# Kernel optimization log

Hardware: AMD Instinct MI355X
Metric: run time of the kernel (lower is better)

## Reference

```python
import jax, jax.numpy as jnp
import numpy as np


def _diag_perm(h, w):
    # Matches torch loop: offsets -(h-1)..w-1, within offset ordered by row i.
    ii, jj = np.meshgrid(np.arange(h), np.arange(w), indexing='ij')
    idx = np.lexsort((ii.ravel(), (jj - ii).ravel())).astype(np.int32)
    inv = np.argsort(idx).astype(np.int32)
    return jnp.asarray(idx), jnp.asarray(inv)


def _mamba(tok, ln_g, ln_b, Win, conv_w, conv_b, Wx, Wdt, bdt, A_log, Dp, Wout):
    # tok: (B, L, C). MambaLayer = LayerNorm + standard Mamba block.
    di, dc = conv_w.shape
    ds = A_log.shape[-1]
    dtr = Wdt.shape[-1]
    mu = tok.mean(-1, keepdims=True)
    var = ((tok - mu) ** 2).mean(-1, keepdims=True)
    t = (tok - mu) * jax.lax.rsqrt(var + 1e-5) * ln_g + ln_b
    xz = jnp.einsum('blc,ec->ble', t, Win)          # (B,L,2*di)
    xh, z = jnp.split(xz, 2, axis=-1)
    # causal depthwise conv over sequence
    xc = jnp.transpose(xh, (0, 2, 1))               # (B,di,L)
    xc = jax.lax.conv_general_dilated(
        xc, conv_w[:, None, :], (1,), [(dc - 1, 0)],
        dimension_numbers=('NCH', 'OIH', 'NCH'), feature_group_count=di)
    u = jax.nn.silu(jnp.transpose(xc, (0, 2, 1)) + conv_b)  # (B,L,di)
    proj = jnp.einsum('bld,ed->ble', u, Wx)
    dt_r, Bm, Cm = jnp.split(proj, [dtr, dtr + ds], axis=-1)
    dt = jax.nn.softplus(jnp.einsum('blr,dr->bld', dt_r, Wdt) + bdt)  # (B,L,di)
    A = -jnp.exp(A_log)                              # (di,ds)

    def step(h, inp):
        dt_t, B_t, C_t, u_t = inp                    # (B,di) (B,ds) (B,ds) (B,di)
        dA = jnp.exp(dt_t[..., None] * A)            # (B,di,ds)
        h = dA * h + dt_t[..., None] * B_t[:, None, :] * u_t[..., None]
        y = jnp.einsum('bds,bs->bd', h, C_t)
        return h, y

    h0 = jnp.zeros((u.shape[0], di, ds), u.dtype)
    _, ys = jax.lax.scan(step, h0, (jnp.moveaxis(dt, 1, 0), jnp.moveaxis(Bm, 1, 0),
                                    jnp.moveaxis(Cm, 1, 0), jnp.moveaxis(u, 1, 0)))
    y = jnp.moveaxis(ys, 0, 1) + u * Dp              # (B,L,di)
    y = y * jax.nn.silu(z)
    return jnp.einsum('bld,cd->blc', y, Wout)


def _forward(x, ln_g, ln_b, Win, conv_w, conv_b, Wx, Wdt, bdt, A_log, Dp, Wout):
    b, c, h, w = x.shape
    idx, inv = _diag_perm(h, w)

    def mam(d, tok):
        return _mamba(tok, ln_g[d], ln_b[d], Win[d], conv_w[d], conv_b[d],
                      Wx[d], Wdt[d], bdt[d], A_log[d], Dp[d], Wout[d])

    row_tok = x.reshape(b, c, h * w).transpose(0, 2, 1)
    row_feat = mam(0, row_tok).transpose(0, 2, 1).reshape(b, c, h, w)
    col_tok = x.transpose(0, 1, 3, 2).reshape(b, c, w * h).transpose(0, 2, 1)
    col_feat = mam(1, col_tok).transpose(0, 2, 1).reshape(b, c, w, h).transpose(0, 1, 3, 2)
    diag_feat = mam(2, row_tok[:, idx, :])[:, inv, :].transpose(0, 2, 1).reshape(b, c, h, w)
    xf = x[:, :, :, ::-1]
    anti_tok = xf.reshape(b, c, h * w).transpose(0, 2, 1)[:, idx, :]
    anti_feat = mam(3, anti_tok)[:, inv, :].transpose(0, 2, 1).reshape(b, c, h, w)[:, :, :, ::-1]
    gate = jax.nn.sigmoid((row_feat + col_feat + diag_feat + anti_feat) / 4.0)
    return x * gate


def setup_inputs() -> dict:
    key = jax.random.key(0)
    ks = jax.random.split(key, 8)
    B, C, H, W = 4, 96, 48, 48
    DI, DS, DC, DTR = 192, 16, 4, 6
    s = 0.05
    return {
        'x': jax.random.normal(ks[0], (B, C, H, W), jnp.float32),
        'ln_g': jnp.ones((4, C), jnp.float32),
        'ln_b': jnp.zeros((4, C), jnp.float32),
        'Win': jax.random.normal(ks[1], (4, 2 * DI, C), jnp.float32) * s,
        'conv_w': jax.random.normal(ks[2], (4, DI, DC), jnp.float32) * s,
        'conv_b': jnp.zeros((4, DI), jnp.float32),
        'Wx': jax.random.normal(ks[3], (4, DTR + 2 * DS, DI), jnp.float32) * s,
        'Wdt': jax.random.normal(ks[4], (4, DI, DTR), jnp.float32) * s,
        'bdt': jax.random.normal(ks[5], (4, DI), jnp.float32) * s,
        'A_log': jnp.log(jnp.broadcast_to(jnp.arange(1, DS + 1, dtype=jnp.float32), (4, DI, DS))),
        'Dp': jnp.ones((4, DI), jnp.float32),
        'Wout': jax.random.normal(ks[6], (4, C, DI), jnp.float32) * s,
    }


def reference(x, ln_g, ln_b, Win, conv_w, conv_b, Wx, Wdt, bdt, A_log, Dp, Wout):
    return _forward(x, ln_g, ln_b, Win, conv_w, conv_b, Wx, Wdt, bdt, A_log, Dp, Wout)
```

## Files before the change

kernel.cpp:

```cpp
#include <hip/hip_runtime.h>
#include <math.h>

#define LSEQ 2304
#define LC 32
#define NCH 72

typedef unsigned short u16;
typedef unsigned int u32;
typedef __attribute__((ext_vector_type(8))) short bf16x8;
typedef __attribute__((ext_vector_type(4))) float f32x4;

__device__ __forceinline__ float sigmoidf_(float v){ return 1.f/(1.f+__expf(-v)); }
__device__ __forceinline__ u16 f2b(float f){
  union{float f; u32 u;} v; v.f = f;
  u32 r = v.u + 0x7fffu + ((v.u >> 16) & 1u);
  return (u16)(r >> 16);
}
__device__ __forceinline__ float b2f(u16 h){
  union{u32 u; float f;} v; v.u = ((u32)h) << 16; return v.f;
}
__device__ __forceinline__ u16 f2h(float f){
  _Float16 h = (_Float16)f;
  union{_Float16 h; u16 u;} v; v.h = h; return v.u;
}
__device__ __forceinline__ float h2f(u16 u){
  union{u16 u; _Float16 h;} v; v.u = u; return (float)v.h;
}
__device__ __forceinline__ uint2 pack4(float a, float b, float c, float d){
  uint2 o;
  o.x = (u32)f2b(a) | ((u32)f2b(b) << 16);
  o.y = (u32)f2b(c) | ((u32)f2b(d) << 16);
  return o;
}
__device__ __forceinline__ float softplus_(float v){
  return fmaxf(v, 0.f) + __logf(1.f + __expf(-fabsf(v)));
}

__global__ void g_kernel(int* __restrict__ g, int* __restrict__ flag){
  int tid = threadIdx.x;
  if (tid == 0) *flag = 1;
  for (int l = tid; l < LSEQ; l += 256){
    g[l] = l;
    g[LSEQ + l] = (l % 48) * 48 + l / 48;
  }
  for (int p = tid; p < LSEQ; p += 256){
    int i = p / 48, j = p % 48, dd = j - i;
    int off = (dd <= 0) ? (47 + dd) * (48 + dd) / 2
                        : 1176 + 48 * (dd - 1) - dd * (dd - 1) / 2;
    int l = off + min(i, j);
    g[2 * LSEQ + l] = p;
  }
  __syncthreads();
  for (int l = tid; l < LSEQ; l += 256){
    int p2 = g[2 * LSEQ + l];
    g[3 * LSEQ + l] = (p2 / 48) * 48 + 47 - (p2 % 48);
  }
}

__global__ void prep_fold(const float* __restrict__ Win, const float* __restrict__ ln_g,
                          const float* __restrict__ ln_b, const float* __restrict__ A_log,
                          const float* __restrict__ Wout, const float* __restrict__ Wx,
                          const float* __restrict__ Wdt, const float* __restrict__ bdt,
                          u16* __restrict__ WinMF, float* __restrict__ b2,
                          float* __restrict__ Aneg2, u16* __restrict__ WoutMF,
                          u16* __restrict__ Wcomb, float* __restrict__ bcomb,
                          int* __restrict__ flag){
  int i = blockIdx.x * 256 + threadIdx.x;
  if (i < 4*192*16){
    float a = -expf(A_log[i]);
    Aneg2[i] = a * 1.44269504f;
    int s = i & 15;
    float a0 = -expf(A_log[i - s]);
    if (fabsf(a - (float)(s + 1) * a0) > 1e-5f * fabsf(a) + 1e-30f)
      atomicAnd(flag, 0);
  }
  if (i < 4*384*96){
    int d = i / 36864, r = i % 36864, c = r % 96;
    WinMF[i] = f2b(Win[i] * ln_g[d*96 + c]);
  }
  if (i < 4*96*192) WoutMF[i] = f2b(Wout[i]);
  if (i < 4*224*192){
    int d = i / 43008, r = i % 43008, e = r / 192, c = r % 192;
    float w;
    if (e < 192){
      const float* wdt = &Wdt[(size_t)(d*192 + e) * 6];
      w = 0.f;
      #pragma unroll
      for (int r6 = 0; r6 < 6; ++r6) w += wdt[r6] * Wx[(size_t)(d*38 + r6) * 192 + c];
    } else if (e < 208){
      w = Wx[(size_t)(d*38 + 6 + (e - 192)) * 192 + c];
    } else {
      w = Wx[(size_t)(d*38 + 22 + (e - 208)) * 192 + c];
    }
    Wcomb[i] = f2b(w);
  }
  if (i < 4*224){
    int d = i / 224, e = i % 224;
    bcomb[i] = (e < 192) ? bdt[d*192 + e] : 0.f;
  }
  if (i < 4*384){
    int d = i / 384;
    const float* wr = &Win[(size_t)i * 96];
    const float* lb = &ln_b[d * 96];
    float s = 0.f;
    for (int c = 0; c < 96; ++c) s += wr[c] * lb[c];
    b2[i] = s;
  }
}

__global__ __launch_bounds__(256) void ln_kernel(const float* __restrict__ x, u16* __restrict__ n){
  __shared__ float red[512];
  int tid = threadIdx.x;
  int s = tid & 63, q = tid >> 6;
  int T = blockIdx.x * 64 + s;
  int b = T / 2304, p = T % 2304;
  const float* xp = x + (size_t)b * 96 * 2304 + p;
  float vals[24];
  float sum = 0.f, ss = 0.f;
  #pragma unroll
  for (int k = 0; k < 24; ++k){
    float v = xp[(size_t)(q*24 + k) * 2304];
    vals[k] = v; sum += v; ss += v*v;
  }
  red[q*64 + s] = sum;
  red[256 + q*64 + s] = ss;
  __syncthreads();
  float S = red[s] + red[64+s] + red[128+s] + red[192+s];
  float Q = red[256+s] + red[320+s] + red[384+s] + red[448+s];
  float mu = S * (1.f/96.f);
  float var = Q * (1.f/96.f) - mu*mu;
  float rs = rsqrtf(var + 1e-5f);
  u32 w[12];
  #pragma unroll
  for (int k = 0; k < 12; ++k){
    float v0 = (vals[2*k]   - mu) * rs;
    float v1 = (vals[2*k+1] - mu) * rs;
    w[k] = (u32)f2b(v0) | ((u32)f2b(v1) << 16);
  }
  uint4* np_ = (uint4*)(n + (size_t)T * 96 + q*24);
  np_[0] = make_uint4(w[0], w[1], w[2],  w[3]);
  np_[1] = make_uint4(w[4], w[5], w[6],  w[7]);
  np_[2] = make_uint4(w[8], w[9], w[10], w[11]);
}

__global__ __launch_bounds__(256) void kproj(const u16* __restrict__ nbf,
    const u16* __restrict__ WinMF, const float* __restrict__ b2,
    u16* __restrict__ xz){
  int d = blockIdx.y;
  int wv = threadIdx.x >> 6, lane = threadIdx.x & 63;
  int lr = lane & 15, lg = lane >> 4;
  int r0 = blockIdx.x * 64 + wv * 16;
  const u16* Ap = nbf + (size_t)(r0 + lr) * 96 + lg * 8;
  bf16x8 tk0 = *(const bf16x8*)(Ap);
  bf16x8 tk1 = *(const bf16x8*)(Ap + 32);
  bf16x8 tk2 = *(const bf16x8*)(Ap + 64);
  const u16* Wb = WinMF + (size_t)d * 36864 + (size_t)lr * 96 + lg * 8;
  const float* b2d = b2 + d * 384;
  u16* out = xz + ((size_t)d * 9216 + r0 + lr) * 384;
  for (int grp = 0; grp < 3; ++grp){
    f32x4 acc[8];
    #pragma unroll
    for (int t = 0; t < 8; ++t)
      acc[t] = *(const f32x4*)&b2d[(grp*8 + t)*16 + lg*4];
    #pragma unroll
    for (int t = 0; t < 8; ++t){
      const u16* wp = Wb + (size_t)(grp*8 + t) * 1536;
      acc[t] = __builtin_amdgcn_mfma_f32_16x16x32_bf16(*(const bf16x8*)(wp     ), tk0, acc[t], 0, 0, 0);
      acc[t] = __builtin_amdgcn_mfma_f32_16x16x32_bf16(*(const bf16x8*)(wp + 32), tk1, acc[t], 0, 0, 0);
      acc[t] = __builtin_amdgcn_mfma_f32_16x16x32_bf16(*(const bf16x8*)(wp + 64), tk2, acc[t], 0, 0, 0);
    }
    #pragma unroll
    for (int t = 0; t < 8; ++t){
      uint2 o = pack4(acc[t][0], acc[t][1], acc[t][2], acc[t][3]);
      *(uint2*)&out[(grp*8 + t)*16 + lg*4] = o;
    }
  }
}

__global__ __launch_bounds__(256) void kconv(const u16* __restrict__ xz, const int* __restrict__ g,
    const float* __restrict__ conv_w, const float* __restrict__ conv_b,
    u16* __restrict__ u, u16* __restrict__ sz){
  __shared__ u16 xh[67][200];
  int d = blockIdx.z, b = blockIdx.y, l0 = blockIdx.x * 64;
  int tid = threadIdx.x;
  const int* gd = g + d * LSEQ;
  const u16* xzd = xz + (size_t)d * 9216 * 384 + (size_t)b * LSEQ * 384;
  for (int i = tid; i < 67*24; i += 256){
    int lt = i / 24, j = i % 24;
    int gl = l0 - 3 + lt;
    uint4 v = make_uint4(0u, 0u, 0u, 0u);
    if (gl >= 0){
      int p = gd[gl];
      v = *(const uint4*)(xzd + (size_t)p * 384 + j * 8);
    }
    *(uint4*)&xh[lt][j*8] = v;
  }
  size_t obase = ((size_t)(d*4 + b) * LSEQ + l0) * 192;
  for (int i = tid; i < 64*48; i += 256){
    int lt = i / 48, j = (i % 48) * 4;
    int p = gd[l0 + lt];
    uint2 zv = *(const uint2*)(xzd + (size_t)p * 384 + 192 + j);
    float z0 = b2f((u16)(zv.x & 0xffff)), z1 = b2f((u16)(zv.x >> 16));
    float z2 = b2f((u16)(zv.y & 0xffff)), z3 = b2f((u16)(zv.y >> 16));
    z0 *= sigmoidf_(z0); z1 *= sigmoidf_(z1); z2 *= sigmoidf_(z2); z3 *= sigmoidf_(z3);
    *(uint2*)(sz + obase + (size_t)lt * 192 + j) = pack4(z0, z1, z2, z3);
  }
  __syncthreads();
  for (int i = tid; i < 64*48; i += 256){
    int lt = i / 48, j = (i % 48) * 4;
    float a0 = conv_b[d*192 + j + 0];
    float a1 = conv_b[d*192 + j + 1];
    float a2 = conv_b[d*192 + j + 2];
    float a3 = conv_b[d*192 + j + 3];
    const float4 w0 = *(const float4*)&conv_w[(size_t)(d*192 + j + 0) * 4];
    const float4 w1 = *(const float4*)&conv_w[(size_t)(d*192 + j + 1) * 4];
    const float4 w2 = *(const float4*)&conv_w[(size_t)(d*192 + j + 2) * 4];
    const float4 w3 = *(const float4*)&conv_w[(size_t)(d*192 + j + 3) * 4];
    const float* w0p = (const float*)&w0;
    const float* w1p = (const float*)&w1;
    const float* w2p = (const float*)&w2;
    const float* w3p = (const float*)&w3;
    #pragma unroll
    for (int kk = 0; kk < 4; ++kk){
      uint2 xv = *(const uint2*)&xh[lt + kk][j];
      a0 += w0p[kk] * b2f((u16)(xv.x & 0xffff));
      a1 += w1p[kk] * b2f((u16)(xv.x >> 16));
      a2 += w2p[kk] * b2f((u16)(xv.y & 0xffff));
      a3 += w3p[kk] * b2f((u16)(xv.y >> 16));
    }
    a0 *= sigmoidf_(a0); a1 *= sigmoidf_(a1); a2 *= sigmoidf_(a2); a3 *= sigmoidf_(a3);
    *(uint2*)(u + obase + (size_t)lt * 192 + j) = pack4(a0, a1, a2, a3);
  }
}

__global__ __launch_bounds__(256) void kernBM(const u16* __restrict__ u,
    const u16* __restrict__ Wcomb, const float* __restrict__ bcomb,
    u16* __restrict__ dtb, float* __restrict__ Bm, float* __restrict__ Cm){
  __shared__ u16 ush[64 * 200];
  int d = blockIdx.y;
  int tid = threadIdx.x;
  int tile0 = blockIdx.x * 64;
  const u16* ub = u + ((size_t)d * 4 * LSEQ + tile0) * 192;
  for (int i = tid; i < 64*24; i += 256){
    int row = i / 24, c8 = i % 24;
    *(uint4*)&ush[row*200 + c8*8] = *(const uint4*)&ub[(size_t)row*192 + c8*8];
  }
  __syncthreads();
  int wv = tid >> 6, lane = tid & 63;
  int lr = lane & 15, lg = lane >> 4;
  const u16* urow = &ush[(wv*16 + lr)*200 + lg*8];
  bf16x8 tk[6];
  #pragma unroll
  for (int kc = 0; kc < 6; ++kc) tk[kc] = *(const bf16x8*)(urow + kc*32);
  const u16* Wb = Wcomb + (size_t)d * 224 * 192 + (size_t)lr * 192 + lg * 8;
  bf16x8 bw[2][6];
  #pragma unroll
  for (int kc = 0; kc < 6; ++kc) bw[0][kc] = *(const bf16x8*)(Wb + kc*32);
  size_t tokrow = (size_t)d * 4 * LSEQ + tile0 + wv*16 + lr;
  for (int t = 0; t < 14; ++t){
    int cur = t & 1;
    if (t < 13){
      const u16* wp = Wb + (size_t)(t + 1) * 3072;
      #pragma unroll
      for (int kc = 0; kc < 6; ++kc) bw[cur^1][kc] = *(const bf16x8*)(wp + kc*32);
    }
    f32x4 a = (f32x4){0.f, 0.f, 0.f, 0.f};
    #pragma unroll
    for (int kc = 0; kc < 6; ++kc)
      a = __builtin_amdgcn_mfma_f32_16x16x32_bf16(bw[cur][kc], tk[kc], a, 0, 0, 0);
    if (t < 12){
      f32x4 bb = *(const f32x4*)&bcomb[d*224 + t*16 + lg*4];
      float s0 = softplus_(a[0] + bb[0]);
      float s1 = softplus_(a[1] + bb[1]);
      float s2 = softplus_(a[2] + bb[2]);
      float s3 = softplus_(a[3] + bb[3]);
      uint2 o;
      o.x = (u32)f2h(s0) | ((u32)f2h(s1) << 16);
      o.y = (u32)f2h(s2) | ((u32)f2h(s3) << 16);
      *(uint2*)&dtb[tokrow * 192 + t*16 + lg*4] = o;
    } else if (t == 12){
      *(float4*)&Bm[tokrow * 16 + lg*4] = make_float4(a[0], a[1], a[2], a[3]);
    } else {
      *(float4*)&Cm[tokrow * 16 + lg*4] = make_float4(a[0], a[1], a[2], a[3]);
    }
  }
}

__global__ __launch_bounds__(192) void kernC1(const u16* __restrict__ dtb, const u16* __restrict__ u,
    const float* __restrict__ Bm, const float* __restrict__ Cm,
    const float* __restrict__ Aneg2, const int* __restrict__ flag,
    u16* __restrict__ hfin, float* __restrict__ Send, u32* __restrict__ yS){
  __shared__ float Bsh[LC*16];
  __shared__ float Csh[LC*16];
  int ch = blockIdx.x, b = blockIdx.y, d = blockIdx.z;
  int seq = d*4 + b;
  int di = threadIdx.x;
  size_t tb = (size_t)seq * LSEQ + ch * LC;
  const float* bp = Bm + tb * 16;
  const float* cp = Cm + tb * 16;
  for (int i = di; i < LC*16; i += 192){ Bsh[i] = bp[i]; Csh[i] = cp[i]; }
  const u16* dtp = dtb + tb * 192;
  const u16* up  = u   + tb * 192;
  u32* ySp = yS + tb * 192;
  float h[16];
  #pragma unroll
  for (int s = 0; s < 16; ++s) h[s] = 0.f;
  float Sacc = 0.f;
  __syncthreads();
  if (*flag){
    float A2_0 = Aneg2[(d*192 + di) * 16];
    for (int j = 0; j < LC; ++j){
      float dtv = h2f(dtp[j*192 + di]);
      float uv  = b2f(up[j*192 + di]);
      float Bs[16], Cs[16];
      {
        const float4* b4 = (const float4*)&Bsh[j * 16];
        const float4* c4 = (const float4*)&Csh[j * 16];
        #pragma unroll
        for (int q = 0; q < 4; ++q){
          float4 v = b4[q]; Bs[q*4]=v.x; Bs[q*4+1]=v.y; Bs[q*4+2]=v.z; Bs[q*4+3]=v.w;
          float4 w = c4[q]; Cs[q*4]=w.x; Cs[q*4+1]=w.y; Cs[q*4+2]=w.z; Cs[q*4+3]=w.w;
        }
      }
      float dtu = dtv * uv;
      float e1 = __builtin_amdgcn_exp2f(dtv * A2_0);
      float e2 = e1*e1, e4 = e2*e2, e8 = e4*e4;
      float p[8];
      p[0]=e1; p[1]=e2; p[2]=e1*e2; p[3]=e4; p[4]=e1*e4; p[5]=e2*e4; p[6]=p[2]*e4; p[7]=e8;
      float yv = 0.f;
      #pragma unroll
      for (int s = 0; s < 8; ++s){
        h[s] = p[s]*h[s] + dtu*Bs[s];
        yv += h[s]*Cs[s];
        float q = p[s]*e8;
        h[s+8] = q*h[s+8] + dtu*Bs[s+8];
        yv += h[s+8]*Cs[s+8];
      }
      Sacc += dtv;
      ySp[j*192 + di] = (u32)f2h(yv) | ((u32)f2h(Sacc) << 16);
    }
  } else {
    float A2[16];
    {
      const float4* ap = (const float4*)&Aneg2[(d*192 + di) * 16];
      #pragma unroll
      for (int q = 0; q < 4; ++q){ float4 a4 = ap[q]; A2[q*4]=a4.x; A2[q*4+1]=a4.y; A2[q*4+2]=a4.z; A2[q*4+3]=a4.w; }
    }
    for (int j = 0; j < LC; ++j){
      float dtv = h2f(dtp[j*192 + di]);
      float uv  = b2f(up[j*192 + di]);
      float Bs[16], Cs[16];
      {
        const float4* b4 = (const float4*)&Bsh[j * 16];
        const float4* c4 = (const float4*)&Csh[j * 16];
        #pragma unroll
        for (int q = 0; q < 4; ++q){
          float4 v = b4[q]; Bs[q*4]=v.x; Bs[q*4+1]=v.y; Bs[q*4+2]=v.z; Bs[q*4+3]=v.w;
          float4 w = c4[q]; Cs[q*4]=w.x; Cs[q*4+1]=w.y; Cs[q*4+2]=w.z; Cs[q*4+3]=w.w;
        }
      }
      float dtu = dtv * uv;
      float yv = 0.f;
      #pragma unroll
      for (int s = 0; s < 16; ++s){
        h[s] = __builtin_amdgcn_exp2f(dtv * A2[s]) * h[s] + dtu * Bs[s];
        yv += h[s] * Cs[s];
      }
      Sacc += dtv;
      ySp[j*192 + di] = (u32)f2h(yv) | ((u32)f2h(Sacc) << 16);
    }
  }
  u16* hf = &hfin[((size_t)seq * NCH + ch) * 3072 + di * 16];
  uint4 o0, o1;
  o0.x = (u32)f2b(h[0])  | ((u32)f2b(h[1])  << 16);
  o0.y = (u32)f2b(h[2])  | ((u32)f2b(h[3])  << 16);
  o0.z = (u32)f2b(h[4])  | ((u32)f2b(h[5])  << 16);
  o0.w = (u32)f2b(h[6])  | ((u32)f2b(h[7])  << 16);
  o1.x = (u32)f2b(h[8])  | ((u32)f2b(h[9])  << 16);
  o1.y = (u32)f2b(h[10]) | ((u32)f2b(h[11]) << 16);
  o1.z = (u32)f2b(h[12]) | ((u32)f2b(h[13]) << 16);
  o1.w = (u32)f2b(h[14]) | ((u32)f2b(h[15]) << 16);
  *(uint4*)hf = o0;
  *(uint4*)(hf + 8) = o1;
  Send[((size_t)seq * NCH + ch) * 192 + di] = Sacc;
}

__global__ __launch_bounds__(256) void kernC2(const u16* __restrict__ hfin, const float* __restrict__ Send,
    const float* __restrict__ Aneg2, u16* __restrict__ hin){
  int t = blockIdx.x * 256 + threadIdx.x;
  int seq = t / 3072, q = t % 3072;
  int di = q >> 4, s = q & 15;
  int d = seq >> 2;
  float A2 = Aneg2[(d*192 + di)*16 + s];
  float hr = 0.f;
  const u16* hf = hfin + (size_t)seq * NCH * 3072 + q;
  u16* hi = hin + (size_t)seq * NCH * 3072 + q;
  const float* Se = Send + (size_t)seq * NCH * 192 + di;
  for (int ch = 0; ch < NCH; ++ch){
    hi[(size_t)ch * 3072] = f2b(hr);
    hr = b2f(hf[(size_t)ch * 3072]) + __builtin_amdgcn_exp2f(A2 * Se[(size_t)ch * 192]) * hr;
  }
}

__global__ __launch_bounds__(384) void kscan2out(const u32* __restrict__ yS, const u16* __restrict__ u,
    const float* __restrict__ Cm,
    const float* __restrict__ Aneg2, const int* __restrict__ flag, const u16* __restrict__ hin,
    const u16* __restrict__ sz, const float* __restrict__ Dp,
    const u16* __restrict__ WoutMF, const int* __restrict__ g,
    u16* __restrict__ feat){
  __shared__ float Csh[64*16];
  __shared__ u16 vsh[64][200];
  int b = blockIdx.y, d = blockIdx.z;
  int seq = d*4 + b;
  int l0 = blockIdx.x * 64;
  int tid = threadIdx.x;
  int gc = tid / 192, di = tid % 192;
  int ch = blockIdx.x * 2 + gc;
  {
    const float* cp = Cm + ((size_t)seq * LSEQ + l0) * 16;
    for (int i = tid; i < 64*16; i += 384) Csh[i] = cp[i];
  }
  float hs[16];
  {
    const uint4* hi4 = (const uint4*)&hin[((size_t)seq * NCH + ch) * 3072 + di * 16];
    uint4 v0 = hi4[0], v1 = hi4[1];
    hs[0]=b2f((u16)(v0.x&0xffff)); hs[1]=b2f((u16)(v0.x>>16));
    hs[2]=b2f((u16)(v0.y&0xffff)); hs[3]=b2f((u16)(v0.y>>16));
    hs[4]=b2f((u16)(v0.z&0xffff)); hs[5]=b2f((u16)(v0.z>>16));
    hs[6]=b2f((u16)(v0.w&0xffff)); hs[7]=b2f((u16)(v0.w>>16));
    hs[8]=b2f((u16)(v1.x&0xffff)); hs[9]=b2f((u16)(v1.x>>16));
    hs[10]=b2f((u16)(v1.y&0xffff)); hs[11]=b2f((u16)(v1.y>>16));
    hs[12]=b2f((u16)(v1.z&0xffff)); hs[13]=b2f((u16)(v1.z>>16));
    hs[14]=b2f((u16)(v1.w&0xffff)); hs[15]=b2f((u16)(v1.w>>16));
  }
  float Dpv = Dp[d*192 + di];
  size_t tb = (size_t)seq * LSEQ + ch * LC;
  const u32* ySp = yS + tb * 192;
  const u16* up  = u   + tb * 192;
  const u16* szp = sz  + tb * 192;
  __syncthreads();
  if (*flag){
    float A2_0 = Aneg2[(d*192 + di) * 16];
    for (int j = 0; j < LC; ++j){
      u32 ys = ySp[j*192 + di];
      float yv = h2f((u16)(ys & 0xffff));
      float Sc = h2f((u16)(ys >> 16));
      float uv  = b2f(up[j*192 + di]);
      float Cs[16];
      {
        const float4* c4 = (const float4*)&Csh[(gc*32 + j) * 16];
        #pragma unroll
        for (int q = 0; q < 4; ++q){ float4 w = c4[q]; Cs[q*4]=w.x; Cs[q*4+1]=w.y; Cs[q*4+2]=w.z; Cs[q*4+3]=w.w; }
      }
      float e1 = __builtin_amdgcn_exp2f(Sc * A2_0);
      float e2 = e1*e1, e4 = e2*e2, e8 = e4*e4;
      float p[8];
      p[0]=e1; p[1]=e2; p[2]=e1*e2; p[3]=e4; p[4]=e1*e4; p[5]=e2*e4; p[6]=p[2]*e4; p[7]=e8;
      float corr = 0.f;
      #pragma unroll
      for (int s = 0; s < 8; ++s){
        corr += p[s]     * hs[s]   * Cs[s];
        corr += p[s]*e8  * hs[s+8] * Cs[s+8];
      }
      float szv = b2f(szp[j*192 + di]);
      vsh[gc*32 + j][di] = f2b((yv + corr + uv * Dpv) * szv);
    }
  } else {
    float A2[16];
    {
      const float4* ap = (const float4*)&Aneg2[(d*192 + di) * 16];
      #pragma unroll
      for (int q = 0; q < 4; ++q){ float4 a4 = ap[q]; A2[q*4]=a4.x; A2[q*4+1]=a4.y; A2[q*4+2]=a4.z; A2[q*4+3]=a4.w; }
    }
    for (int j = 0; j < LC; ++j){
      u32 ys = ySp[j*192 + di];
      float yv = h2f((u16)(ys & 0xffff));
      float Sc = h2f((u16)(ys >> 16));
      float uv  = b2f(up[j*192 + di]);
      float Cs[16];
      {
        const float4* c4 = (const float4*)&Csh[(gc*32 + j) * 16];
        #pragma unroll
        for (int q = 0; q < 4; ++q){ float4 w = c4[q]; Cs[q*4]=w.x; Cs[q*4+1]=w.y; Cs[q*4+2]=w.z; Cs[q*4+3]=w.w; }
      }
      float corr = 0.f;
      #pragma unroll
      for (int s = 0; s < 16; ++s)
        corr += __builtin_amdgcn_exp2f(Sc * A2[s]) * hs[s] * Cs[s];
      float szv = b2f(szp[j*192 + di]);
      vsh[gc*32 + j][di] = f2b((yv + corr + uv * Dpv) * szv);
    }
  }
  __syncthreads();
  if (tid < 256){
    int wv = tid >> 6, lane = tid & 63;
    int lr = lane & 15, lg = lane >> 4;
    bf16x8 tk[6];
    #pragma unroll
    for (int kc = 0; kc < 6; ++kc)
      tk[kc] = *(const bf16x8*)&vsh[wv*16 + lr][kc*32 + lg*8];
    const u16* Wb = WoutMF + (size_t)d * 18432 + (size_t)lr * 192 + lg * 8;
    f32x4 acc[6];
    #pragma unroll
    for (int t = 0; t < 6; ++t) acc[t] = (f32x4){0.f, 0.f, 0.f, 0.f};
    #pragma unroll
    for (int t = 0; t < 6; ++t){
      const u16* wp = Wb + (size_t)t * 3072;
      #pragma unroll
      for (int kc = 0; kc < 6; ++kc)
        acc[t] = __builtin_amdgcn_mfma_f32_16x16x32_bf16(*(const bf16x8*)(wp + kc*32), tk[kc], acc[t], 0, 0, 0);
    }
    u16* fd = feat + (size_t)seq * LSEQ * 96;
    int p = g[d*LSEQ + l0 + wv*16 + lr];
    #pragma unroll
    for (int t = 0; t < 6; ++t){
      uint2 o = pack4(acc[t][0], acc[t][1], acc[t][2], acc[t][3]);
      *(uint2*)&fd[(size_t)p * 96 + t*16 + lg*4] = o;
    }
  }
}

__global__ __launch_bounds__(256) void kernE(const float* __restrict__ x, const u16* __restrict__ feat,
    float* __restrict__ out){
  __shared__ float acc[64 * 97];
  int p0 = blockIdx.x * 64, b = blockIdx.y;
  int tid = threadIdx.x;
  const size_t DS_ = (size_t)4 * LSEQ * 96;
  size_t base = ((size_t)b * LSEQ + p0) * 96;
  for (int i = tid; i < 3072; i += 256){
    int pp = i / 48, c2 = (i % 48) * 2;
    size_t o = base + (size_t)pp * 96 + c2;
    u32 v0 = *(const u32*)(feat + o);
    u32 v1 = *(const u32*)(feat + DS_ + o);
    u32 v2 = *(const u32*)(feat + 2*DS_ + o);
    u32 v3 = *(const u32*)(feat + 3*DS_ + o);
    float s0 = b2f((u16)(v0 & 0xffff)) + b2f((u16)(v1 & 0xffff)) + b2f((u16)(v2 & 0xffff)) + b2f((u16)(v3 & 0xffff));
    float s1 = b2f((u16)(v0 >> 16)) + b2f((u16)(v1 >> 16)) + b2f((u16)(v2 >> 16)) + b2f((u16)(v3 >> 16));
    acc[pp*97 + c2] = s0;
    acc[pp*97 + c2 + 1] = s1;
  }
  __syncthreads();
  for (int i = tid; i < 6144; i += 256){
    int c = i / 64, pp = i % 64;
    size_t o = ((size_t)b * 96 + c) * LSEQ + p0 + pp;
    out[o] = x[o] * sigmoidf_(acc[pp*97 + c] * 0.25f);
  }
}

extern "C" void kernel_launch(void* const* d_in, const int* in_sizes, int n_in,
                              void* d_out, int out_size, void* d_ws, size_t ws_size,
                              hipStream_t stream) {
  const float* x      = (const float*)d_in[0];
  const float* ln_g   = (const float*)d_in[1];
  const float* ln_b   = (const float*)d_in[2];
  const float* Win    = (const float*)d_in[3];
  const float* conv_w = (const float*)d_in[4];
  const float* conv_b = (const float*)d_in[5];
  const float* Wx     = (const float*)d_in[6];
  const float* Wdt    = (const float*)d_in[7];
  const float* bdt    = (const float*)d_in[8];
  const float* A_log  = (const float*)d_in[9];
  const float* Dp     = (const float*)d_in[10];
  const float* Wout   = (const float*)d_in[11];

  char* W = (char*)d_ws;
  char* W0 = W;
  auto alloc = [&](size_t bytes) -> char* {
    char* p = W; W += (bytes + 255) & ~(size_t)255; return p;
  };
  int*   g      = (int*)  alloc((size_t)4 * LSEQ * 4);
  int*   flag   = (int*)  alloc(256);
  float* Aneg2  = (float*)alloc((size_t)4 * 192 * 16 * 4);
  float* b2     = (float*)alloc((size_t)4 * 384 * 4);
  u16*   WinMF  = (u16*)  alloc((size_t)4 * 384 * 96 * 2);
  u16*   WoutMF = (u16*)  alloc((size_t)4 * 96 * 192 * 2);
  u16*   Wcomb  = (u16*)  alloc((size_t)4 * 224 * 192 * 2);
  float* bcomb  = (float*)alloc((size_t)4 * 224 * 4);
  u16*   nbf    = (u16*)  alloc((size_t)9216 * 96 * 2);
  u16*   xz     = (u16*)  alloc((size_t)4 * 9216 * 384 * 2);
  u16*   ubf    = (u16*)  alloc((size_t)16 * LSEQ * 192 * 2);
  u16*   szbf   = (u16*)  alloc((size_t)16 * LSEQ * 192 * 2);
  u16*   dtb    = (u16*)  alloc((size_t)16 * LSEQ * 192 * 2);
  float* Bm     = (float*)alloc((size_t)16 * LSEQ * 16 * 4);
  float* Cm     = (float*)alloc((size_t)16 * LSEQ * 16 * 4);
  u32*   ySbuf  = (u32*)  alloc((size_t)16 * LSEQ * 192 * 4);
  float* Send   = (float*)alloc((size_t)16 * NCH * 192 * 4);
  u16*   hfin   = (u16*)  alloc((size_t)16 * NCH * 3072 * 2);
  u16*   hin    = (u16*)  alloc((size_t)16 * NCH * 3072 * 2);
  u16*   feat   = (u16*)  alloc((size_t)16 * LSEQ * 96 * 2);
  if ((size_t)(W - W0) > ws_size) return;

  g_kernel<<<1, 256, 0, stream>>>(g, flag);
  prep_fold<<<768, 256, 0, stream>>>(Win, ln_g, ln_b, A_log, Wout, Wx, Wdt, bdt,
                                     WinMF, b2, Aneg2, WoutMF, Wcomb, bcomb, flag);
  ln_kernel<<<144, 256, 0, stream>>>(x, nbf);
  kproj<<<dim3(144, 4), 256, 0, stream>>>(nbf, WinMF, b2, xz);
  kconv<<<dim3(36, 4, 4), 256, 0, stream>>>(xz, g, conv_w, conv_b, ubf, szbf);
  kernBM<<<dim3(144, 4), 256, 0, stream>>>(ubf, Wcomb, bcomb, dtb, Bm, Cm);
  kernC1<<<dim3(NCH, 4, 4), 192, 0, stream>>>(dtb, ubf, Bm, Cm, Aneg2, flag, hfin, Send, ySbuf);
  kernC2<<<192, 256, 0, stream>>>(hfin, Send, Aneg2, hin);
  kscan2out<<<dim3(36, 4, 4), 384, 0, stream>>>(ySbuf, ubf, Cm, Aneg2, flag, hin, szbf, Dp,
                                                WoutMF, g, feat);
  kernE<<<dim3(36, 4), 256, 0, stream>>>(x, feat, (float*)d_out);
}
```

Measured before the change: 199.1 us.

## Fold index-table kernel into prep, stage scan inputs in LDS, batch loads

Removes the single-block index-table kernel by computing the permutation tables inside prep_fold, and replaces the flag init with a memset using inverted flag semantics. kernC1 now copies the chunk's dt and u values into shared memory with 16-byte vector loads before the recurrence. kernC2 and kscan2out group their global loads in batches of eight so more memory requests are in flight before the dependent arithmetic runs. The added shared memory in kernC1 may lower occupancy.

```diff
diff --git a/kernel.cpp b/kernel.cpp
--- a/kernel.cpp
+++ b/kernel.cpp
@@ -34,27 +34,6 @@
 }
 __device__ __forceinline__ float softplus_(float v){
   return fmaxf(v, 0.f) + __logf(1.f + __expf(-fabsf(v)));
-}
-
-__global__ void g_kernel(int* __restrict__ g, int* __restrict__ flag){
-  int tid = threadIdx.x;
-  if (tid == 0) *flag = 1;
-  for (int l = tid; l < LSEQ; l += 256){
-    g[l] = l;
-    g[LSEQ + l] = (l % 48) * 48 + l / 48;
-  }
-  for (int p = tid; p < LSEQ; p += 256){
-    int i = p / 48, j = p % 48, dd = j - i;
-    int off = (dd <= 0) ? (47 + dd) * (48 + dd) / 2
-                        : 1176 + 48 * (dd - 1) - dd * (dd - 1) / 2;
-    int l = off + min(i, j);
-    g[2 * LSEQ + l] = p;
-  }
-  __syncthreads();
-  for (int l = tid; l < LSEQ; l += 256){
-    int p2 = g[2 * LSEQ + l];
-    g[3 * LSEQ + l] = (p2 / 48) * 48 + 47 - (p2 % 48);
-  }
 }
 
 __global__ void prep_fold(const float* __restrict__ Win, const float* __restrict__ ln_g,
@@ -64,15 +43,27 @@
                           u16* __restrict__ WinMF, float* __restrict__ b2,
                           float* __restrict__ Aneg2, u16* __restrict__ WoutMF,
                           u16* __restrict__ Wcomb, float* __restrict__ bcomb,
-                          int* __restrict__ flag){
+                          int* __restrict__ g, int* __restrict__ flag){
   int i = blockIdx.x * 256 + threadIdx.x;
+  if (i < LSEQ){
+    int l = i;
+    g[l] = l;
+    g[LSEQ + l] = (l % 48) * 48 + l / 48;
+    int p = i;
+    int ii = p / 48, jj = p % 48, dd = jj - ii;
+    int off = (dd <= 0) ? (47 + dd) * (48 + dd) / 2
+                        : 1176 + 48 * (dd - 1) - dd * (dd - 1) / 2;
+    int l2 = off + min(ii, jj);
+    g[2 * LSEQ + l2] = p;
+    g[3 * LSEQ + l2] = ii * 48 + 47 - jj;
+  }
   if (i < 4*192*16){
     float a = -expf(A_log[i]);
     Aneg2[i] = a * 1.44269504f;
     int s = i & 15;
     float a0 = -expf(A_log[i - s]);
     if (fabsf(a - (float)(s + 1) * a0) > 1e-5f * fabsf(a) + 1e-30f)
-      atomicAnd(flag, 0);
+      atomicOr(flag, 1);
   }
   if (i < 4*384*96){
     int d = i / 36864, r = i % 36864, c = r % 96;
@@ -292,6 +283,8 @@
     u16* __restrict__ hfin, float* __restrict__ Send, u32* __restrict__ yS){
   __shared__ float Bsh[LC*16];
   __shared__ float Csh[LC*16];
+  __shared__ u16 dtsh[LC*192];
+  __shared__ u16 ush2[LC*192];
   int ch = blockIdx.x, b = blockIdx.y, d = blockIdx.z;
   int seq = d*4 + b;
   int di = threadIdx.x;
@@ -299,19 +292,26 @@
   const float* bp = Bm + tb * 16;
   const float* cp = Cm + tb * 16;
   for (int i = di; i < LC*16; i += 192){ Bsh[i] = bp[i]; Csh[i] = cp[i]; }
-  const u16* dtp = dtb + tb * 192;
-  const u16* up  = u   + tb * 192;
+  {
+    const uint4* dt4 = (const uint4*)(dtb + tb * 192);
+    const uint4* u4  = (const uint4*)(u   + tb * 192);
+    #pragma unroll
+    for (int i = di; i < 768; i += 192){
+      *(uint4*)&dtsh[i*8] = dt4[i];
+      *(uint4*)&ush2[i*8] = u4[i];
+    }
+  }
   u32* ySp = yS + tb * 192;
   float h[16];
   #pragma unroll
   for (int s = 0; s < 16; ++s) h[s] = 0.f;
   float Sacc = 0.f;
   __syncthreads();
-  if (*flag){
+  if (*flag == 0){
     float A2_0 = Aneg2[(d*192 + di) * 16];
     for (int j = 0; j < LC; ++j){
-      float dtv = h2f(dtp[j*192 + di]);
-      float uv  = b2f(up[j*192 + di]);
+      float dtv = h2f(dtsh[j*192 + di]);
+      float uv  = b2f(ush2[j*192 + di]);
       float Bs[16], Cs[16];
       {
         const float4* b4 = (const float4*)&Bsh[j * 16];
@@ -347,8 +347,8 @@
       for (int q = 0; q < 4; ++q){ float4 a4 = ap[q]; A2[q*4]=a4.x; A2[q*4+1]=a4.y; A2[q*4+2]=a4.z; A2[q*4+3]=a4.w; }
     }
     for (int j = 0; j < LC; ++j){
-      float dtv = h2f(dtp[j*192 + di]);
-      float uv  = b2f(up[j*192 + di]);
+      float dtv = h2f(dtsh[j*192 + di]);
+      float uv  = b2f(ush2[j*192 + di]);
       float Bs[16], Cs[16];
       {
         const float4* b4 = (const float4*)&Bsh[j * 16];
@@ -396,9 +396,18 @@
   const u16* hf = hfin + (size_t)seq * NCH * 3072 + q;
   u16* hi = hin + (size_t)seq * NCH * 3072 + q;
   const float* Se = Send + (size_t)seq * NCH * 192 + di;
-  for (int ch = 0; ch < NCH; ++ch){
-    hi[(size_t)ch * 3072] = f2b(hr);
-    hr = b2f(hf[(size_t)ch * 3072]) + __builtin_amdgcn_exp2f(A2 * Se[(size_t)ch * 192]) * hr;
+  for (int ch = 0; ch < NCH; ch += 8){
+    float Se8[8]; u16 hf8[8];
+    #pragma unroll
+    for (int k = 0; k < 8; ++k){
+      Se8[k] = Se[(size_t)(ch+k) * 192];
+      hf8[k] = hf[(size_t)(ch+k) * 3072];
+    }
+    #pragma unroll
+    for (int k = 0; k < 8; ++k){
+      hi[(size_t)(ch+k) * 3072] = f2b(hr);
+      hr = b2f(hf8[k]) + __builtin_amdgcn_exp2f(A2 * Se8[k]) * hr;
+    }
   }
 }
 
@@ -439,31 +448,43 @@
   const u16* up  = u   + tb * 192;
   const u16* szp = sz  + tb * 192;
   __syncthreads();
-  if (*flag){
+  if (*flag == 0){
     float A2_0 = Aneg2[(d*192 + di) * 16];
-    for (int j = 0; j < LC; ++j){
-      u32 ys = ySp[j*192 + di];
-      float yv = h2f((u16)(ys & 0xffff));
-      float Sc = h2f((u16)(ys >> 16));
-      float uv  = b2f(up[j*192 + di]);
-      float Cs[16];
-      {
-        const float4* c4 = (const float4*)&Csh[(gc*32 + j) * 16];
+    #pragma unroll
+    for (int jb = 0; jb < 4; ++jb){
+      u32 ys8[8]; u16 uu8[8], zz8[8];
+      #pragma unroll
+      for (int k = 0; k < 8; ++k){
+        int j = jb*8 + k;
+        ys8[k] = ySp[j*192 + di];
+        uu8[k] = up[j*192 + di];
+        zz8[k] = szp[j*192 + di];
+      }
+      #pragma unroll
+      for (int k = 0; k < 8; ++k){
+        int j = jb*8 + k;
+        float yv = h2f((u16)(ys8[k] & 0xffff));
+        float Sc = h2f((u16)(ys8[k] >> 16));
+        float uv = b2f(uu8[k]);
+        float Cs[16];
+        {
+          const float4* c4 = (const float4*)&Csh[(gc*32 + j) * 16];
+          #pragma unroll
+          for (int q = 0; q < 4; ++q){ float4 w = c4[q]; Cs[q*4]=w.x; Cs[q*4+1]=w.y; Cs[q*4+2]=w.z; Cs[q*4+3]=w.w; }
+        }
+        float e1 = __builtin_amdgcn_exp2f(Sc * A2_0);
+        float e2 = e1*e1, e4 = e2*e2, e8 = e4*e4;
+        float p[8];
+        p[0]=e1; p[1]=e2; p[2]=e1*e2; p[3]=e4; p[4]=e1*e4; p[5]=e2*e4; p[6]=p[2]*e4; p[7]=e8;
+        float corr = 0.f;
         #pragma unroll
-        for (int q = 0; q < 4; ++q){ float4 w = c4[q]; Cs[q*4]=w.x; Cs[q*4+1]=w.y; Cs[q*4+2]=w.z; Cs[q*4+3]=w.w; }
-      }
-      float e1 = __builtin_amdgcn_exp2f(Sc * A2_0);
-      float e2 = e1*e1, e4 = e2*e2, e8 = e4*e4;
-      float p[8];
-      p[0]=e1; p[1]=e2; p[2]=e1*e2; p[3]=e4; p[4]=e1*e4; p[5]=e2*e4; p[6]=p[2]*e4; p[7]=e8;
-      float corr = 0.f;
-      #pragma unroll
-      for (int s = 0; s < 8; ++s){
-        corr += p[s]     * hs[s]   * Cs[s];
-        corr += p[s]*e8  * hs[s+8] * Cs[s+8];
-      }
-      float szv = b2f(szp[j*192 + di]);
-      vsh[gc*32 + j][di] = f2b((yv + corr + uv * Dpv) * szv);
+        for (int s = 0; s < 8; ++s){
+          corr += p[s]    * hs[s]   * Cs[s];
+          corr += p[s]*e8 * hs[s+8] * Cs[s+8];
+        }
+        float szv = b2f(zz8[k]);
+        vsh[gc*32 + j][di] = f2b((yv + corr + uv * Dpv) * szv);
+      }
     }
   } else {
     float A2[16];
@@ -472,23 +493,35 @@
       #pragma unroll
       for (int q = 0; q < 4; ++q){ float4 a4 = ap[q]; A2[q*4]=a4.x; A2[q*4+1]=a4.y; A2[q*4+2]=a4.z; A2[q*4+3]=a4.w; }
     }
-    for (int j = 0; j < LC; ++j){
-      u32 ys = ySp[j*192 + di];
-      float yv = h2f((u16)(ys & 0xffff));
-      float Sc = h2f((u16)(ys >> 16));
-      float uv  = b2f(up[j*192 + di]);
-      float Cs[16];
-      {
-        const float4* c4 = (const float4*)&Csh[(gc*32 + j) * 16];
+    #pragma unroll
+    for (int jb = 0; jb < 4; ++jb){
+      u32 ys8[8]; u16 uu8[8], zz8[8];
+      #pragma unroll
+      for (int k = 0; k < 8; ++k){
+        int j = jb*8 + k;
+        ys8[k] = ySp[j*192 + di];
+        uu8[k] = up[j*192 + di];
+        zz8[k] = szp[j*192 + di];
+      }
+      #pragma unroll
+      for (int k = 0; k < 8; ++k){
+        int j = jb*8 + k;
+        float yv = h2f((u16)(ys8[k] & 0xffff));
+        float Sc = h2f((u16)(ys8[k] >> 16));
+        float uv = b2f(uu8[k]);
+        float Cs[16];
+        {
+          const float4* c4 = (const float4*)&Csh[(gc*32 + j) * 16];
+          #pragma unroll
+          for (int q = 0; q < 4; ++q){ float4 w = c4[q]; Cs[q*4]=w.x; Cs[q*4+1]=w.y; Cs[q*4+2]=w.z; Cs[q*4+3]=w.w; }
+        }
+        float corr = 0.f;
         #pragma unroll
-        for (int q = 0; q < 4; ++q){ float4 w = c4[q]; Cs[q*4]=w.x; Cs[q*4+1]=w.y; Cs[q*4+2]=w.z; Cs[q*4+3]=w.w; }
-      }
-      float corr = 0.f;
-      #pragma unroll
-      for (int s = 0; s < 16; ++s)
-        corr += __builtin_amdgcn_exp2f(Sc * A2[s]) * hs[s] * Cs[s];
-      float szv = b2f(szp[j*192 + di]);
-      vsh[gc*32 + j][di] = f2b((yv + corr + uv * Dpv) * szv);
+        for (int s = 0; s < 16; ++s)
+          corr += __builtin_amdgcn_exp2f(Sc * A2[s]) * hs[s] * Cs[s];
+        float szv = b2f(zz8[k]);
+        vsh[gc*32 + j][di] = f2b((yv + corr + uv * Dpv) * szv);
+      }
     }
   }
   __syncthreads();
@@ -590,9 +623,9 @@
   u16*   feat   = (u16*)  alloc((size_t)16 * LSEQ * 96 * 2);
   if ((size_t)(W - W0) > ws_size) return;
 
-  g_kernel<<<1, 256, 0, stream>>>(g, flag);
+  hipMemsetAsync(flag, 0, sizeof(int), stream);
   prep_fold<<<768, 256, 0, stream>>>(Win, ln_g, ln_b, A_log, Wout, Wx, Wdt, bdt,
-                                     WinMF, b2, Aneg2, WoutMF, Wcomb, bcomb, flag);
+                                     WinMF, b2, Aneg2, WoutMF, Wcomb, bcomb, g, flag);
   ln_kernel<<<144, 256, 0, stream>>>(x, nbf);
   kproj<<<dim3(144, 4), 256, 0, stream>>>(nbf, WinMF, b2, xz);
   kconv<<<dim3(36, 4, 4), 256, 0, stream>>>(xz, g, conv_w, conv_b, ubf, szbf);
```

Result: faster. 190.5 us (-4.3%).
